# Performance work log

Hardware: AMD Instinct MI355X
Metric: run time of the kernel (lower is better)

The kernel has to match this reference:

```python
import math
import jax, jax.numpy as jnp
import numpy as np

B, T, C, H = 2, 2048, 1024, 16
HD = C // H  # head dim = 64


def setup_inputs() -> dict:
    key = jax.random.key(0)
    k1, k2, k3 = jax.random.split(key, 3)
    x = jax.random.normal(k1, (B, T, C), dtype=jnp.float32)
    w_attn = jax.random.normal(k2, (C, 3 * C), dtype=jnp.float32) * (1.0 / math.sqrt(C))
    b_attn = jnp.zeros((3 * C,), dtype=jnp.float32)
    w_proj = jax.random.normal(k3, (C, C), dtype=jnp.float32) * (1.0 / math.sqrt(C))
    b_proj = jnp.zeros((C,), dtype=jnp.float32)
    return {"x": x, "w_attn": w_attn, "b_attn": b_attn, "w_proj": w_proj, "b_proj": b_proj}


def reference(x, w_attn, b_attn, w_proj, b_proj):
    b, t, c = x.shape
    hd = c // H
    # fused QKV projection: [B,T,3C]
    qkv = x @ w_attn + b_attn
    q, k, v = jnp.split(qkv, 3, axis=2)
    # [B,T,C] -> [B,H,T,hd]
    q = q.reshape(b, t, H, hd).transpose(0, 2, 1, 3)
    k = k.reshape(b, t, H, hd).transpose(0, 2, 1, 3)
    v = v.reshape(b, t, H, hd).transpose(0, 2, 1, 3)
    # scaled scores: [B,H,T,T]
    att = jnp.einsum("bhqd,bhkd->bhqk", q, k) * (1.0 / math.sqrt(hd))
    # causal mask: keep lower triangle, -inf elsewhere
    causal = jnp.tril(jnp.ones((t, t), dtype=bool))
    att = jnp.where(causal[None, None, :, :], att, jnp.float32(-jnp.inf))
    att = jax.nn.softmax(att, axis=-1)
    # attention-weighted values: [B,H,T,hd] -> [B,T,C]
    y = jnp.einsum("bhqk,bhkd->bhqd", att, v)
    y = y.transpose(0, 2, 1, 3).reshape(b, t, c)
    # output projection (dropout prob 0 => identity)
    return y @ w_proj + b_proj
```

## Files before the change

### kernel.cpp

```cpp
#include <hip/hip_runtime.h>
#include <type_traits>


typedef __bf16 bf16x8 __attribute__((ext_vector_type(8)));
typedef __bf16 bf16x4 __attribute__((ext_vector_type(4)));
typedef short shortx4 __attribute__((ext_vector_type(4)));
typedef float f32x4 __attribute__((ext_vector_type(4)));

#define B_ 2
#define T_ 2048
#define C_ 1024
#define H_ 16
#define HD_ 64
#define ROWS_ (B_ * T_)
#define N3C_ (3 * C_)

__device__ inline void gll16(const void* g, void* l) {
    __builtin_amdgcn_global_load_lds(
        (const __attribute__((address_space(1))) void*)g,
        (__attribute__((address_space(3))) void*)l, 16, 0, 0);
}

__device__ inline f32x4 mfma16x16x16(bf16x4 a, bf16x4 b, f32x4 c) {
#if defined(__HIP_DEVICE_COMPILE__)
#if __has_builtin(__builtin_amdgcn_mfma_f32_16x16x16bf16_1k)
    return __builtin_amdgcn_mfma_f32_16x16x16bf16_1k(
        __builtin_bit_cast(shortx4, a), __builtin_bit_cast(shortx4, b), c, 0, 0, 0);
#else
    return __builtin_amdgcn_mfma_f32_16x16x16_bf16(
        __builtin_bit_cast(shortx4, a), __builtin_bit_cast(shortx4, b), c, 0, 0, 0);
#endif
#else
    (void)a; (void)b;
    return c;
#endif
}

__device__ inline float v_exp2(float x) {
#if defined(__HIP_DEVICE_COMPILE__)
    float r;
    asm("v_exp_f32 %0, %1" : "=v"(r) : "v"(x));
    return r;
#else
    return x;
#endif
}

__device__ inline float bias_at(const void* bias, int col, bool in_bf) {
    return in_bf ? (float)((const __bf16*)bias)[col] : ((const float*)bias)[col];
}

__global__ void detect_dtype(const unsigned* __restrict__ w, unsigned* __restrict__ flag) {
    int lane = threadIdx.x & 63;
    int cnt = 0;
#pragma unroll
    for (int i = 0; i < 4; ++i) {
        unsigned v = w[lane * 4 + i];
        unsigned e = (v >> 7) & 0xFFu;
        cnt += (e >= 116u && e <= 134u) ? 1 : 0;
    }
#pragma unroll
    for (int off = 1; off < 64; off <<= 1) cnt += __shfl_xor(cnt, off, 64);
    if (lane == 0) *flag = (cnt >= 128) ? 1u : 0u;
}

__global__ __launch_bounds__(256) void convert_to_bf16(const void* __restrict__ src,
                                                       __bf16* __restrict__ dst, int n,
                                                       const unsigned* __restrict__ flag) {
    bool isbf = (*flag != 0u);
    int i = (blockIdx.x * 256 + threadIdx.x) * 8;
    if (i >= n) return;
    if (isbf) {
        *(bf16x8*)&dst[i] = *(const bf16x8*)((const __bf16*)src + i);
    } else {
        const float4* s4 = (const float4*)src;
        float4 a = s4[i / 4], b = s4[i / 4 + 1];
        bf16x8 v;
        v[0] = (__bf16)a.x; v[1] = (__bf16)a.y; v[2] = (__bf16)a.z; v[3] = (__bf16)a.w;
        v[4] = (__bf16)b.x; v[5] = (__bf16)b.y; v[6] = (__bf16)b.z; v[7] = (__bf16)b.w;
        *(bf16x8*)&dst[i] = v;
    }
}

__global__ __launch_bounds__(256) void transpose2(const void* __restrict__ wa,
                                                  __bf16* __restrict__ wat,
                                                  const void* __restrict__ wp,
                                                  __bf16* __restrict__ wpt,
                                                  const unsigned* __restrict__ flag) {
    int z = blockIdx.z;
    if (z && blockIdx.x >= 16) return;
    const void* src = z ? wp : wa;
    __bf16* dst = z ? wpt : wat;
    int R = C_, Cc = z ? C_ : N3C_;

    __shared__ __align__(16) __bf16 tile[64][65];
    bool isbf = (*flag != 0u);
    const __bf16* sb = (const __bf16*)src;
    const float* sf = (const float*)src;
    int cb = blockIdx.x * 64, rb = blockIdx.y * 64;
    for (int i = threadIdx.x; i < 4096; i += 256) {
        int r = i >> 6, c = i & 63;
        size_t idx = (size_t)(rb + r) * Cc + cb + c;
        tile[r][c] = isbf ? sb[idx] : (__bf16)sf[idx];
    }
    __syncthreads();
    for (int i = threadIdx.x; i < 4096; i += 256) {
        int r = i >> 6, c = i & 63;
        dst[(size_t)(cb + r) * R + rb + c] = tile[c][r];
    }
}

__global__ __launch_bounds__(256) void gemm_qkv(const __bf16* __restrict__ A,
                                                const __bf16* __restrict__ Bt,
                                                const void* __restrict__ bias,
                                                __bf16* __restrict__ qg,
                                                __bf16* __restrict__ kg,
                                                __bf16* __restrict__ vtg,
                                                const unsigned* __restrict__ flag) {
    const int K = C_;
    __shared__ __align__(16) __bf16 As[128 * 32];
    __shared__ __align__(16) __bf16 Bs[128 * 32];
    bool in_bf = (*flag != 0u);
    int tid = threadIdx.x;
    int wave = tid >> 6, lane = tid & 63;
    int quad = lane >> 4, l15 = lane & 15;
    int mb = blockIdx.y * 128, nb = blockIdx.x * 128;
    int wm = (wave >> 1) * 64, wn = (wave & 1) * 64;

    f32x4 acc[4][4] = {};

    for (int k0 = 0; k0 < K; k0 += 32) {
        __syncthreads();
#pragma unroll
        for (int q = 0; q < 2; ++q) {
            int id = q * 256 + tid;
            int r = id >> 2, c8 = (id & 3) * 8;
            gll16(&A[(size_t)(mb + r) * K + k0 + c8], &As[(q * 256 + wave * 64) * 8]);
            gll16(&Bt[(size_t)(nb + r) * K + k0 + c8], &Bs[(q * 256 + wave * 64) * 8]);
        }
        __syncthreads();

        bf16x8 af[4], bfr[4];
#pragma unroll
        for (int i = 0; i < 4; ++i)
            af[i] = *(const bf16x8*)&As[(wm + i * 16 + l15) * 32 + quad * 8];
#pragma unroll
        for (int j = 0; j < 4; ++j)
            bfr[j] = *(const bf16x8*)&Bs[(wn + j * 16 + l15) * 32 + quad * 8];
#pragma unroll
        for (int i = 0; i < 4; ++i)
#pragma unroll
            for (int j = 0; j < 4; ++j)
                acc[i][j] = __builtin_amdgcn_mfma_f32_16x16x32_bf16(af[i], bfr[j], acc[i][j], 0, 0, 0);
    }

#pragma unroll
    for (int i = 0; i < 4; ++i) {
        int row = mb + wm + i * 16 + quad * 4;
#pragma unroll
        for (int j = 0; j < 4; ++j) {
            int col = nb + wn + j * 16 + l15;
            float bv = bias_at(bias, col, in_bf);
            int region = col >> 10;
            int cc = col & 1023;
            int hh = cc >> 6, hd = cc & 63;
#pragma unroll
            for (int r = 0; r < 4; ++r) {
                int rr = row + r;
                int t = rr & (T_ - 1), bb = rr >> 11;
                float val = acc[i][j][r] + bv;
                size_t bh = (size_t)(bb * H_ + hh);
                if (region == 0)      qg[(bh * T_ + t) * HD_ + hd] = (__bf16)val;
                else if (region == 1) kg[(bh * T_ + t) * HD_ + hd] = (__bf16)val;
                else                  vtg[(bh * HD_ + hd) * T_ + t] = (__bf16)val;
            }
        }
    }
}

__global__ __launch_bounds__(256) void attn_kernel(const __bf16* __restrict__ qg,
                                                   const __bf16* __restrict__ kg,
                                                   const __bf16* __restrict__ vtg,
                                                   __bf16* __restrict__ y) {
    const int LDT = 72;
    __shared__ __align__(16) __bf16 Ks[64 * LDT];
    __shared__ __align__(16) __bf16 Vts[64 * LDT];

    int tid = threadIdx.x, wave = tid >> 6, lane = tid & 63;
    int quad = lane >> 4, l15 = lane & 15;
    int p = blockIdx.x;
    int qA = p, qB = 31 - p;
    int bh = blockIdx.y;
    int b = bh >> 4, h = bh & 15;

    const __bf16* qbh = qg + (size_t)bh * T_ * HD_;
    const __bf16* kbh = kg + (size_t)bh * T_ * HD_;
    const __bf16* vbh = vtg + (size_t)bh * HD_ * T_;

    int rowA = qA * 64 + wave * 16;
    int rowB = qB * 64 + wave * 16;

    bf16x8 qfA[2], qfB[2];
#pragma unroll
    for (int ks = 0; ks < 2; ++ks) {
        qfA[ks] = *(const bf16x8*)&qbh[(size_t)(rowA + l15) * HD_ + ks * 32 + quad * 8];
        qfB[ks] = *(const bf16x8*)&qbh[(size_t)(rowB + l15) * HD_ + ks * 32 + quad * 8];
    }

    f32x4 oA[4] = {}, oB[4] = {};
    f32x4 laccA = {}, laccB = {};
    const float C1 = 0.125f * 1.44269504088896340736f;
    const float C2 = 12.0f * 1.44269504088896340736f;

    bf16x4 onesb;
#pragma unroll
    for (int e = 0; e < 4; ++e) onesb[e] = (__bf16)1.0f;

    bf16x8 kf[4][2];
    bf16x4 vf[4][4];

    auto tile_step = [&](auto diagc, const bf16x8* qf, int rowX, int kbase,
                         f32x4* o, f32x4& lacc) {
        constexpr bool DIAG = decltype(diagc)::value;
        f32x4 s[4] = {};
#pragma unroll
        for (int ks = 0; ks < 2; ++ks)
#pragma unroll
            for (int j = 0; j < 4; ++j)
                s[j] = __builtin_amdgcn_mfma_f32_16x16x32_bf16(kf[j][ks], qf[ks], s[j], 0, 0, 0);

        int q = rowX + l15;
#pragma unroll
        for (int j = 0; j < 4; ++j) {
            bf16x4 pb;
#pragma unroll
            for (int r = 0; r < 4; ++r) {
                float e = v_exp2(fmaf(s[j][r], C1, -C2));
                if (DIAG) {
                    int key = kbase + j * 16 + quad * 4 + r;
                    e = (key > q) ? 0.f : e;
                }
                pb[r] = (__bf16)e;
            }
#pragma unroll
            for (int i = 0; i < 4; ++i)
                o[i] = mfma16x16x16(pb, vf[i][j], o[i]);
            lacc = mfma16x16x16(pb, onesb, lacc);
        }
    };

    for (int kt = 0; kt <= qB; ++kt) {
        int kbase = kt * 64;
        __syncthreads();
#pragma unroll
        for (int t = 0; t < 2; ++t) {
            int vid = tid + t * 256;
            int r = vid >> 3, c = (vid & 7) * 8;
            *(bf16x8*)&Ks[r * LDT + c]  = *(const bf16x8*)&kbh[(size_t)(kbase + r) * HD_ + c];
            *(bf16x8*)&Vts[r * LDT + c] = *(const bf16x8*)&vbh[(size_t)r * T_ + kbase + c];
        }
        __syncthreads();

#pragma unroll
        for (int j = 0; j < 4; ++j)
#pragma unroll
            for (int ks = 0; ks < 2; ++ks)
                kf[j][ks] = *(const bf16x8*)&Ks[(j * 16 + l15) * LDT + ks * 32 + quad * 8];
#pragma unroll
        for (int i = 0; i < 4; ++i)
#pragma unroll
            for (int j = 0; j < 4; ++j)
                vf[i][j] = *(const bf16x4*)&Vts[(i * 16 + l15) * LDT + j * 16 + quad * 4];

        if (kt == qB) tile_step(std::true_type{},  qfB, rowB, kbase, oB, laccB);
        else          tile_step(std::false_type{}, qfB, rowB, kbase, oB, laccB);
        if (kt < qA)       tile_step(std::false_type{}, qfA, rowA, kbase, oA, laccA);
        else if (kt == qA) tile_step(std::true_type{},  qfA, rowA, kbase, oA, laccA);
    }

#pragma unroll
    for (int i = 0; i < 4; ++i) {
        int col = h * HD_ + i * 16 + l15;
#pragma unroll
        for (int r = 0; r < 4; ++r) {
            y[(size_t)(b * T_ + rowA + quad * 4 + r) * C_ + col] = (__bf16)(oA[i][r] / laccA[r]);
            y[(size_t)(b * T_ + rowB + quad * 4 + r) * C_ + col] = (__bf16)(oB[i][r] / laccB[r]);
        }
    }
}

__global__ __launch_bounds__(256) void gemm_proj(const __bf16* __restrict__ A,
                                                 const __bf16* __restrict__ Bt,
                                                 const void* __restrict__ bias,
                                                 void* __restrict__ Cv,
                                                 const unsigned* __restrict__ flag) {
    const int K = C_, N = C_;
    __shared__ __align__(16) __bf16 As[64 * 32];
    __shared__ __align__(16) __bf16 Bs[128 * 32];
    bool in_bf = (*flag != 0u);
    int tid = threadIdx.x;
    int wave = tid >> 6, lane = tid & 63;
    int quad = lane >> 4, l15 = lane & 15;
    int mb = blockIdx.y * 64, nb = blockIdx.x * 128;
    int wm = (wave >> 1) * 32, wn = (wave & 1) * 64;

    f32x4 acc[2][4] = {};

    for (int k0 = 0; k0 < K; k0 += 32) {
        __syncthreads();
        {
            int r = tid >> 2, c8 = (tid & 3) * 8;
            gll16(&A[(size_t)(mb + r) * K + k0 + c8], &As[(wave * 64) * 8]);
        }
#pragma unroll
        for (int q = 0; q < 2; ++q) {
            int id = q * 256 + tid;
            int r = id >> 2, c8 = (id & 3) * 8;
            gll16(&Bt[(size_t)(nb + r) * K + k0 + c8], &Bs[(q * 256 + wave * 64) * 8]);
        }
        __syncthreads();

        bf16x8 af[2], bfr[4];
#pragma unroll
        for (int i = 0; i < 2; ++i)
            af[i] = *(const bf16x8*)&As[(wm + i * 16 + l15) * 32 + quad * 8];
#pragma unroll
        for (int j = 0; j < 4; ++j)
            bfr[j] = *(const bf16x8*)&Bs[(wn + j * 16 + l15) * 32 + quad * 8];
#pragma unroll
        for (int i = 0; i < 2; ++i)
#pragma unroll
            for (int j = 0; j < 4; ++j)
                acc[i][j] = __builtin_amdgcn_mfma_f32_16x16x32_bf16(af[i], bfr[j], acc[i][j], 0, 0, 0);
    }

#pragma unroll
    for (int i = 0; i < 2; ++i) {
        int row = mb + wm + i * 16 + quad * 4;
#pragma unroll
        for (int j = 0; j < 4; ++j) {
            int col = nb + wn + j * 16 + l15;
            float bv = bias_at(bias, col, in_bf);
#pragma unroll
            for (int r = 0; r < 4; ++r) {
                float val = acc[i][j][r] + bv;
                size_t off = (size_t)(row + r) * N + col;
                if (in_bf) ((__bf16*)Cv)[off] = (__bf16)val;
                else       ((float*)Cv)[off]  = val;
            }
        }
    }
}

extern "C" void kernel_launch(void* const* d_in, const int* in_sizes, int n_in,
                              void* d_out, int out_size, void* d_ws, size_t ws_size,
                              hipStream_t stream) {
    const void* x      = d_in[0];
    const void* w_attn = d_in[1];
    const void* b_attn = d_in[2];
    const void* w_proj = d_in[3];
    const void* b_proj = d_in[4];

    char* base = (char*)d_ws;
    unsigned* flag = (unsigned*)base;
    __bf16* xc   = (__bf16*)(base + 256);
    __bf16* wat  = xc + (size_t)ROWS_ * C_;
    __bf16* wpt  = wat + (size_t)N3C_ * C_;
    __bf16* qg   = wpt + (size_t)C_ * C_;
    __bf16* kg   = qg + (size_t)B_ * H_ * T_ * HD_;
    __bf16* vtg  = kg + (size_t)B_ * H_ * T_ * HD_;
    __bf16* yb   = vtg + (size_t)B_ * H_ * T_ * HD_;

    detect_dtype<<<1, 64, 0, stream>>>((const unsigned*)x, flag);

    convert_to_bf16<<<(ROWS_ * C_ / 8 + 255) / 256, 256, 0, stream>>>(x, xc, ROWS_ * C_, flag);

    transpose2<<<dim3(N3C_ / 64, C_ / 64, 2), 256, 0, stream>>>(w_attn, wat, w_proj, wpt, flag);

    gemm_qkv<<<dim3(N3C_ / 128, ROWS_ / 128), 256, 0, stream>>>(
        xc, wat, b_attn, qg, kg, vtg, flag);

    attn_kernel<<<dim3(16, B_ * H_), 256, 0, stream>>>(qg, kg, vtg, yb);

    gemm_proj<<<dim3(C_ / 128, ROWS_ / 64), 256, 0, stream>>>(yb, wpt, b_proj, d_out, flag);
}
```

Before: 200.9 us.

## Double K-step per barrier in GEMMs and move V transpose to separate kernel

Both GEMM kernels now load a 64-wide K slab per iteration (two 32-wide sub-tiles in doubled LDS buffers), which halves the number of barrier pairs per K loop. The QKV GEMM epilogue now writes V in the same row-major layout as Q and K instead of a strided transposed scatter. A new transpose_v kernel then transposes V through a shared-memory tile with vectorized stores. This trades uncoalesced scattered stores for an extra launch and an extra pass over V, and doubles LDS use per GEMM block, which may lower occupancy.

```diff
diff --git a/kernel.cpp b/kernel.cpp
--- a/kernel.cpp
+++ b/kernel.cpp
@@ -115,11 +115,11 @@
                                                 const void* __restrict__ bias,
                                                 __bf16* __restrict__ qg,
                                                 __bf16* __restrict__ kg,
-                                                __bf16* __restrict__ vtg,
+                                                __bf16* __restrict__ vn,
                                                 const unsigned* __restrict__ flag) {
     const int K = C_;
-    __shared__ __align__(16) __bf16 As[128 * 32];
-    __shared__ __align__(16) __bf16 Bs[128 * 32];
+    __shared__ __align__(16) __bf16 As[2 * 128 * 32];
+    __shared__ __align__(16) __bf16 Bs[2 * 128 * 32];
     bool in_bf = (*flag != 0u);
     int tid = threadIdx.x;
     int wave = tid >> 6, lane = tid & 63;
@@ -129,29 +129,33 @@
 
     f32x4 acc[4][4] = {};
 
-    for (int k0 = 0; k0 < K; k0 += 32) {
-        __syncthreads();
-#pragma unroll
-        for (int q = 0; q < 2; ++q) {
-            int id = q * 256 + tid;
-            int r = id >> 2, c8 = (id & 3) * 8;
-            gll16(&A[(size_t)(mb + r) * K + k0 + c8], &As[(q * 256 + wave * 64) * 8]);
-            gll16(&Bt[(size_t)(nb + r) * K + k0 + c8], &Bs[(q * 256 + wave * 64) * 8]);
-        }
-        __syncthreads();
-
-        bf16x8 af[4], bfr[4];
-#pragma unroll
-        for (int i = 0; i < 4; ++i)
-            af[i] = *(const bf16x8*)&As[(wm + i * 16 + l15) * 32 + quad * 8];
-#pragma unroll
-        for (int j = 0; j < 4; ++j)
-            bfr[j] = *(const bf16x8*)&Bs[(wn + j * 16 + l15) * 32 + quad * 8];
-#pragma unroll
-        for (int i = 0; i < 4; ++i)
+    for (int k0 = 0; k0 < K; k0 += 64) {
+        __syncthreads();
+#pragma unroll
+        for (int q = 0; q < 4; ++q) {
+            int kh = q >> 1;
+            int idx = (q & 1) * 256 + tid;
+            int r = idx >> 2, c32 = (idx & 3) * 8;
+            gll16(&A[(size_t)(mb + r) * K + k0 + kh * 32 + c32], &As[(q * 256 + wave * 64) * 8]);
+            gll16(&Bt[(size_t)(nb + r) * K + k0 + kh * 32 + c32], &Bs[(q * 256 + wave * 64) * 8]);
+        }
+        __syncthreads();
+
+#pragma unroll
+        for (int ks = 0; ks < 2; ++ks) {
+            bf16x8 af[4], bfr[4];
+#pragma unroll
+            for (int i = 0; i < 4; ++i)
+                af[i] = *(const bf16x8*)&As[ks * 4096 + (wm + i * 16 + l15) * 32 + quad * 8];
 #pragma unroll
             for (int j = 0; j < 4; ++j)
-                acc[i][j] = __builtin_amdgcn_mfma_f32_16x16x32_bf16(af[i], bfr[j], acc[i][j], 0, 0, 0);
+                bfr[j] = *(const bf16x8*)&Bs[ks * 4096 + (wn + j * 16 + l15) * 32 + quad * 8];
+#pragma unroll
+            for (int i = 0; i < 4; ++i)
+#pragma unroll
+                for (int j = 0; j < 4; ++j)
+                    acc[i][j] = __builtin_amdgcn_mfma_f32_16x16x32_bf16(af[i], bfr[j], acc[i][j], 0, 0, 0);
+        }
     }
 
 #pragma unroll
@@ -164,17 +168,38 @@
             int region = col >> 10;
             int cc = col & 1023;
             int hh = cc >> 6, hd = cc & 63;
+            __bf16* dstbase = (region == 0) ? qg : (region == 1) ? kg : vn;
 #pragma unroll
             for (int r = 0; r < 4; ++r) {
                 int rr = row + r;
                 int t = rr & (T_ - 1), bb = rr >> 11;
                 float val = acc[i][j][r] + bv;
                 size_t bh = (size_t)(bb * H_ + hh);
-                if (region == 0)      qg[(bh * T_ + t) * HD_ + hd] = (__bf16)val;
-                else if (region == 1) kg[(bh * T_ + t) * HD_ + hd] = (__bf16)val;
-                else                  vtg[(bh * HD_ + hd) * T_ + t] = (__bf16)val;
+                dstbase[(bh * T_ + t) * HD_ + hd] = (__bf16)val;
             }
         }
+    }
+}
+
+__global__ __launch_bounds__(256) void transpose_v(const __bf16* __restrict__ vn,
+                                                   __bf16* __restrict__ vtg) {
+    __shared__ __align__(16) __bf16 tile[64][65];
+    int bh = blockIdx.y, t0 = blockIdx.x * 64;
+    const __bf16* src = vn + ((size_t)bh * T_ + t0) * HD_;
+    __bf16* dst = vtg + (size_t)bh * HD_ * T_ + t0;
+    int tid = threadIdx.x;
+    int r = tid >> 3, c = (tid & 7) * 8;
+    *(bf16x8*)&tile[r][c] = *(const bf16x8*)&src[(size_t)r * HD_ + c];
+    *(bf16x8*)&tile[r + 32][c] = *(const bf16x8*)&src[(size_t)(r + 32) * HD_ + c];
+    __syncthreads();
+#pragma unroll
+    for (int it = 0; it < 2; ++it) {
+        int idx = it * 256 + tid;
+        int hd = idx >> 3, ch = (idx & 7) * 8;
+        bf16x8 v;
+#pragma unroll
+        for (int e = 0; e < 8; ++e) v[e] = tile[ch + e][hd];
+        *(bf16x8*)&dst[(size_t)hd * T_ + ch] = v;
     }
 }
 
@@ -295,8 +320,8 @@
                                                  void* __restrict__ Cv,
                                                  const unsigned* __restrict__ flag) {
     const int K = C_, N = C_;
-    __shared__ __align__(16) __bf16 As[64 * 32];
-    __shared__ __align__(16) __bf16 Bs[128 * 32];
+    __shared__ __align__(16) __bf16 As[2 * 64 * 32];
+    __shared__ __align__(16) __bf16 Bs[2 * 128 * 32];
     bool in_bf = (*flag != 0u);
     int tid = threadIdx.x;
     int wave = tid >> 6, lane = tid & 63;
@@ -306,32 +331,37 @@
 
     f32x4 acc[2][4] = {};
 
-    for (int k0 = 0; k0 < K; k0 += 32) {
-        __syncthreads();
-        {
-            int r = tid >> 2, c8 = (tid & 3) * 8;
-            gll16(&A[(size_t)(mb + r) * K + k0 + c8], &As[(wave * 64) * 8]);
-        }
+    for (int k0 = 0; k0 < K; k0 += 64) {
+        __syncthreads();
 #pragma unroll
         for (int q = 0; q < 2; ++q) {
-            int id = q * 256 + tid;
-            int r = id >> 2, c8 = (id & 3) * 8;
-            gll16(&Bt[(size_t)(nb + r) * K + k0 + c8], &Bs[(q * 256 + wave * 64) * 8]);
-        }
-        __syncthreads();
-
-        bf16x8 af[2], bfr[4];
-#pragma unroll
-        for (int i = 0; i < 2; ++i)
-            af[i] = *(const bf16x8*)&As[(wm + i * 16 + l15) * 32 + quad * 8];
-#pragma unroll
-        for (int j = 0; j < 4; ++j)
-            bfr[j] = *(const bf16x8*)&Bs[(wn + j * 16 + l15) * 32 + quad * 8];
-#pragma unroll
-        for (int i = 0; i < 2; ++i)
+            int r = tid >> 2, c32 = (tid & 3) * 8;
+            gll16(&A[(size_t)(mb + r) * K + k0 + q * 32 + c32], &As[(q * 256 + wave * 64) * 8]);
+        }
+#pragma unroll
+        for (int q = 0; q < 4; ++q) {
+            int kh = q >> 1;
+            int idx = (q & 1) * 256 + tid;
+            int r = idx >> 2, c32 = (idx & 3) * 8;
+            gll16(&Bt[(size_t)(nb + r) * K + k0 + kh * 32 + c32], &Bs[(q * 256 + wave * 64) * 8]);
+        }
+        __syncthreads();
+
+#pragma unroll
+        for (int ks = 0; ks < 2; ++ks) {
+            bf16x8 af[2], bfr[4];
+#pragma unroll
+            for (int i = 0; i < 2; ++i)
+                af[i] = *(const bf16x8*)&As[ks * 2048 + (wm + i * 16 + l15) * 32 + quad * 8];
 #pragma unroll
             for (int j = 0; j < 4; ++j)
-                acc[i][j] = __builtin_amdgcn_mfma_f32_16x16x32_bf16(af[i], bfr[j], acc[i][j], 0, 0, 0);
+                bfr[j] = *(const bf16x8*)&Bs[ks * 4096 + (wn + j * 16 + l15) * 32 + quad * 8];
+#pragma unroll
+            for (int i = 0; i < 2; ++i)
+#pragma unroll
+                for (int j = 0; j < 4; ++j)
+                    acc[i][j] = __builtin_amdgcn_mfma_f32_16x16x32_bf16(af[i], bfr[j], acc[i][j], 0, 0, 0);
+        }
     }
 
 #pragma unroll
@@ -368,7 +398,8 @@
     __bf16* wpt  = wat + (size_t)N3C_ * C_;
     __bf16* qg   = wpt + (size_t)C_ * C_;
     __bf16* kg   = qg + (size_t)B_ * H_ * T_ * HD_;
-    __bf16* vtg  = kg + (size_t)B_ * H_ * T_ * HD_;
+    __bf16* vn   = kg + (size_t)B_ * H_ * T_ * HD_;
+    __bf16* vtg  = vn + (size_t)B_ * H_ * T_ * HD_;
     __bf16* yb   = vtg + (size_t)B_ * H_ * T_ * HD_;
 
     detect_dtype<<<1, 64, 0, stream>>>((const unsigned*)x, flag);
@@ -378,7 +409,9 @@
     transpose2<<<dim3(N3C_ / 64, C_ / 64, 2), 256, 0, stream>>>(w_attn, wat, w_proj, wpt, flag);
 
     gemm_qkv<<<dim3(N3C_ / 128, ROWS_ / 128), 256, 0, stream>>>(
-        xc, wat, b_attn, qg, kg, vtg, flag);
+        xc, wat, b_attn, qg, kg, vn, flag);
+
+    transpose_v<<<dim3(T_ / 64, B_ * H_), 256, 0, stream>>>(vn, vtg);
 
     attn_kernel<<<dim3(16, B_ * H_), 256, 0, stream>>>(qg, kg, vtg, yb);
 
```

After: 195.1 us. -2.9%, faster.
